# Performance work log

Measured on AMD Instinct MI355X. Metric: run time of the kernel, lower is better.

The kernel has to match this reference:

```python
import jax, jax.numpy as jnp
import numpy as np

DROPOUT = 0.1      # ban radius in normalized coords
INVALID = -2.0     # PositionGetter.INVALID sentinel
EPS = 1e-08


def setup_inputs() -> dict:
    key = jax.random.key(0)
    k1, k2, k3 = jax.random.split(key, 3)
    B, C, T, D = 64, 275, 3000, 2
    x = jax.random.normal(k1, (B, C, T), dtype=jnp.float32)
    positions = jax.random.uniform(k2, (B, C, D), dtype=jnp.float32)
    # row 0: the ban center applied to x; rows 1..100: Monte-Carlo test centers
    centers = jax.random.uniform(k3, (101, D), dtype=jnp.float32)
    return {"x": x, "positions": positions, "centers": centers}


def reference(x, positions, centers):
    # valid_mask: channel is valid unless all coords equal the INVALID sentinel
    valid = ~jnp.all(positions == INVALID, axis=-1)          # [B, C] bool
    x = x * valid[..., None].astype(x.dtype)
    # distances from every channel position to every center, all at once
    # centers: [N, D], positions: [B, C, D] -> dist: [N, B, C]
    diff = positions[None, :, :, :] - centers[:, None, None, :]
    dist = jnp.linalg.norm(diff, axis=-1)                    # [N, B, C]
    kept_all = (dist > DROPOUT) | (~valid)[None]             # [N, B, C] bool
    # apply the actual ban (first center)
    x = x * kept_all[0][..., None].astype(x.dtype)
    # Monte-Carlo keep probability over the remaining 100 centers
    prob_kept = jnp.mean(kept_all[1:].astype(x.dtype), axis=0)  # [B, C]
    return x / (prob_kept[..., None] + EPS)
```

## Files before the change

kernel.cpp:

```cpp
#include <hip/hip_runtime.h>
#include <math.h>


__global__ __launch_bounds__(256) void ChannelDropout_14851996910142_kernel(
    const float* __restrict__ x,
    const float* __restrict__ pos,
    const float* __restrict__ centers,
    float* __restrict__ out,
    int ncenters, int tlen)
{
    const int row = blockIdx.x;
    const int tid = threadIdx.x;
    __shared__ float s_scale;

    if (tid < 64) {
        const float px = pos[2 * row];
        const float py = pos[2 * row + 1];
        const bool valid = !(px == -2.0f && py == -2.0f);

        float cnt = 0.0f;
        for (int c = 1 + tid; c < ncenters; c += 64) {
            const float dx = px - centers[2 * c];
            const float dy = py - centers[2 * c + 1];
            const float d2 = __fadd_rn(__fmul_rn(dx, dx), __fmul_rn(dy, dy));
            const float d = sqrtf(d2);
            cnt += (d > 0.1f) ? 1.0f : 0.0f;
        }
        #pragma unroll
        for (int off = 32; off > 0; off >>= 1)
            cnt += __shfl_down(cnt, off, 64);

        if (tid == 0) {
            const float dx0 = px - centers[0];
            const float dy0 = py - centers[1];
            const float d02 = __fadd_rn(__fmul_rn(dx0, dx0), __fmul_rn(dy0, dy0));
            const bool kept0 = sqrtf(d02) > 0.1f;
            const float prob = cnt / (float)(ncenters - 1);
            s_scale = (valid && kept0) ? (1.0f / (prob + 1e-8f)) : 0.0f;
        }
    }
    __syncthreads();
    const float s = s_scale;

    const size_t base = (size_t)row * (size_t)tlen;
    const int t4 = tlen >> 2;
    const float4* __restrict__ xr = (const float4*)(x + base);
    float4* __restrict__ orow = (float4*)(out + base);
    for (int i = tid; i < t4; i += 256) {
        float4 v = xr[i];
        v.x *= s; v.y *= s; v.z *= s; v.w *= s;
        orow[i] = v;
    }
    for (int i = (t4 << 2) + tid; i < tlen; i += 256) {
        out[base + i] = x[base + i] * s;
    }
}

extern "C" void kernel_launch(void* const* d_in, const int* in_sizes, int n_in,
                              void* d_out, int out_size, void* d_ws, size_t ws_size,
                              hipStream_t stream) {
    const float* x       = (const float*)d_in[0];
    const float* pos     = (const float*)d_in[1];
    const float* centers = (const float*)d_in[2];
    float* out = (float*)d_out;

    const int rows     = in_sizes[1] / 2;
    const int tlen     = in_sizes[0] / rows;
    const int ncenters = in_sizes[2] / 2;

    ChannelDropout_14851996910142_kernel<<<rows, 256, 0, stream>>>(
        x, pos, centers, out, ncenters, tlen);
}
```

Measured before the change: 350.6 us.

## Prefetch row data before computing scale; per-wave redundant reduction; nontemporal stores

Each thread now issues its x loads for the row (up to three float4s) before computing the Monte-Carlo keep probability. This overlaps memory latency with the distance computation. Every wavefront computes the scale redundantly with xor shuffles, which removes the shared-memory broadcast and the __syncthreads barrier. Output is written with nontemporal stores to avoid cache pollution, at the cost of extra registers and duplicated center math per wave.

Measured after the change: 358.3 us. +2.2%, slower.

```diff
diff --git a/kernel.cpp b/kernel.cpp
--- a/kernel.cpp
+++ b/kernel.cpp
@@ -1,6 +1,8 @@
 #include <hip/hip_runtime.h>
 #include <math.h>
 
+
+typedef float f32x4 __attribute__((ext_vector_type(4)));
 
 __global__ __launch_bounds__(256) void ChannelDropout_14851996910142_kernel(
     const float* __restrict__ x,
@@ -9,47 +11,51 @@
     float* __restrict__ out,
     int ncenters, int tlen)
 {
-    const int row = blockIdx.x;
-    const int tid = threadIdx.x;
-    __shared__ float s_scale;
-
-    if (tid < 64) {
-        const float px = pos[2 * row];
-        const float py = pos[2 * row + 1];
-        const bool valid = !(px == -2.0f && py == -2.0f);
-
-        float cnt = 0.0f;
-        for (int c = 1 + tid; c < ncenters; c += 64) {
-            const float dx = px - centers[2 * c];
-            const float dy = py - centers[2 * c + 1];
-            const float d2 = __fadd_rn(__fmul_rn(dx, dx), __fmul_rn(dy, dy));
-            const float d = sqrtf(d2);
-            cnt += (d > 0.1f) ? 1.0f : 0.0f;
-        }
-        #pragma unroll
-        for (int off = 32; off > 0; off >>= 1)
-            cnt += __shfl_down(cnt, off, 64);
-
-        if (tid == 0) {
-            const float dx0 = px - centers[0];
-            const float dy0 = py - centers[1];
-            const float d02 = __fadd_rn(__fmul_rn(dx0, dx0), __fmul_rn(dy0, dy0));
-            const bool kept0 = sqrtf(d02) > 0.1f;
-            const float prob = cnt / (float)(ncenters - 1);
-            s_scale = (valid && kept0) ? (1.0f / (prob + 1e-8f)) : 0.0f;
-        }
-    }
-    __syncthreads();
-    const float s = s_scale;
+    const int row  = blockIdx.x;
+    const int tid  = threadIdx.x;
+    const int lane = tid & 63;
 
     const size_t base = (size_t)row * (size_t)tlen;
     const int t4 = tlen >> 2;
-    const float4* __restrict__ xr = (const float4*)(x + base);
-    float4* __restrict__ orow = (float4*)(out + base);
-    for (int i = tid; i < t4; i += 256) {
-        float4 v = xr[i];
-        v.x *= s; v.y *= s; v.z *= s; v.w *= s;
-        orow[i] = v;
+    const f32x4* __restrict__ xr   = (const f32x4*)(x + base);
+    f32x4* __restrict__       orow = (f32x4*)(out + base);
+
+    const int i0 = tid, i1 = tid + 256, i2 = tid + 512;
+    const bool p0 = i0 < t4, p1 = i1 < t4, p2 = i2 < t4;
+    f32x4 v0 = {}, v1 = {}, v2 = {};
+    if (p0) v0 = xr[i0];
+    if (p1) v1 = xr[i1];
+    if (p2) v2 = xr[i2];
+
+    const float px = pos[2 * row];
+    const float py = pos[2 * row + 1];
+    const bool valid = !(px == -2.0f && py == -2.0f);
+
+    float cnt = 0.0f;
+    for (int c = 1 + lane; c < ncenters; c += 64) {
+        const float dx = px - centers[2 * c];
+        const float dy = py - centers[2 * c + 1];
+        const float d2 = __fadd_rn(__fmul_rn(dx, dx), __fmul_rn(dy, dy));
+        cnt += (sqrtf(d2) > 0.1f) ? 1.0f : 0.0f;
+    }
+    #pragma unroll
+    for (int off = 32; off > 0; off >>= 1)
+        cnt += __shfl_xor(cnt, off, 64);
+
+    const float dx0 = px - centers[0];
+    const float dy0 = py - centers[1];
+    const float d02 = __fadd_rn(__fmul_rn(dx0, dx0), __fmul_rn(dy0, dy0));
+    const bool kept0 = sqrtf(d02) > 0.1f;
+    const float prob = cnt / (float)(ncenters - 1);
+    const float s = (valid && kept0) ? (1.0f / (prob + 1e-8f)) : 0.0f;
+
+    if (p0) __builtin_nontemporal_store(v0 * s, orow + i0);
+    if (p1) __builtin_nontemporal_store(v1 * s, orow + i1);
+    if (p2) __builtin_nontemporal_store(v2 * s, orow + i2);
+
+    for (int i = tid + 768; i < t4; i += 256) {
+        f32x4 v = xr[i];
+        __builtin_nontemporal_store(v * s, orow + i);
     }
     for (int i = (t4 << 2) + tid; i < tlen; i += 256) {
         out[base + i] = x[base + i] * s;
```
